# Optimization experiments

Measured on AMD Instinct MI355X. Metric: run time of the kernel, lower is better.

The kernel has to match this reference:

```python
import jax, jax.numpy as jnp
import numpy as np

HEAD_NUM = 8
ATT_DIM = 64
NUM_UNITS = HEAD_NUM * ATT_DIM  # 512
B, T, D = 8, 1024, NUM_UNITS
NEG_BIG = -2.0**32 + 1.0


def _sinusoidal_table(max_len, num_hidden):
    P = np.zeros((1, max_len, num_hidden), dtype=np.float32)
    X = np.arange(max_len, dtype=np.float32).reshape(-1, 1) / np.power(
        10000.0, np.arange(0, num_hidden, 2, dtype=np.float32) / num_hidden)
    P[:, :, 0::2] = np.sin(X)
    P[:, :, 1::2] = np.cos(X)
    return P


def setup_inputs() -> dict:
    key = jax.random.key(0)
    ks = jax.random.split(key, 8)
    w_scale = 0.02
    return {
        "queries": jax.random.normal(ks[0], (B, T, D), dtype=jnp.float32),
        "keys": jax.random.normal(ks[1], (B, T, D), dtype=jnp.float32),
        "query_masks": jnp.ones((B, T), dtype=jnp.float32),
        "key_masks": jnp.ones((B, T), dtype=jnp.float32),
        "pos_table": jnp.asarray(_sinusoidal_table(T, D)),
        "W_Query": jax.random.normal(ks[2], (D, D), dtype=jnp.float32) * w_scale,
        "W_key": jax.random.normal(ks[3], (D, D), dtype=jnp.float32) * w_scale,
        "W_Value": jax.random.normal(ks[4], (D, D), dtype=jnp.float32) * w_scale,
        "fw1": jax.random.normal(ks[5], (D, 4 * D), dtype=jnp.float32) * w_scale,
        "fw2": jax.random.normal(ks[6], (4 * D, D), dtype=jnp.float32) * w_scale,
    }


def reference(queries, keys, query_masks, key_masks, pos_table,
              W_Query, W_key, W_Value, fw1, fw2):
    h, dh = HEAD_NUM, ATT_DIM
    pe_scale = jnp.asarray(NUM_UNITS ** 0.5, dtype=queries.dtype)
    pos = pos_table[:, :queries.shape[1], :] * pe_scale  # scale=True
    q_in = queries + pos
    k_in = keys + pos

    q = jnp.einsum('btd,de->bte', q_in, W_Query)
    k = jnp.einsum('btd,de->bte', k_in, W_key)
    # Faithful to source: values computed from the projected keys.
    v = jnp.einsum('btd,de->bte', k, W_Value)

    # split heads: (B,T,h*dh) -> (h,B,T,dh)
    def heads(x):
        return x.reshape(B, T, h, dh).transpose(2, 0, 1, 3)
    qh, kh, vh = heads(q), heads(k), heads(v)

    scores = jnp.einsum('hbqd,hbkd->hbqk', qh, kh) / (dh ** 0.5)
    # key padding mask
    scores = jnp.where(key_masks[None, :, None, :] == 1.0, scores, NEG_BIG)
    # blinding: mask the diagonal
    eye = jnp.eye(T, dtype=bool)
    scores = jnp.where(eye[None, None, :, :], NEG_BIG, scores)
    attn = jax.nn.softmax(scores, axis=-1)
    attn = attn * query_masks[None, :, :, None]

    out = jnp.einsum('hbqk,hbkd->hbqd', attn, vh)
    result = out.transpose(1, 2, 0, 3).reshape(B, T, D)  # merge heads

    result = result + q_in  # residual (use_res, queries after PE)

    # feed-forward with residual
    hidden = jax.nn.relu(jnp.einsum('btd,df->btf', result, fw1))
    ffn = jnp.einsum('btf,fd->btd', hidden, fw2)
    result = result + ffn

    # output_type == 'mean'
    return jnp.mean(result, axis=1, keepdims=True)  # (B,1,D)
```

## Files before the change

kernel.cpp:

```cpp
#include <hip/hip_runtime.h>


typedef __bf16 bf16x8 __attribute__((ext_vector_type(8)));
typedef __bf16 bf16x4 __attribute__((ext_vector_type(4)));
typedef float f32x4 __attribute__((ext_vector_type(4)));
typedef unsigned short u16x8 __attribute__((ext_vector_type(8)));
typedef unsigned short u16x4 __attribute__((ext_vector_type(4)));

#define MFMA_BF16(a, b, c) __builtin_amdgcn_mfma_f32_16x16x32_bf16((a), (b), (c), 0, 0, 0)
#define NEGBIG (-4294967295.0f)
#define QSCALE 0.18033688011112042f
#define EXP2(x) __builtin_amdgcn_exp2f(x)

#define GLL16(g, l)                                                                 \
    __builtin_amdgcn_global_load_lds((__attribute__((address_space(1))) void*)(g),  \
                                     (__attribute__((address_space(3))) void*)(l),  \
                                     16, 0, 0)

static __device__ __forceinline__ unsigned short f2bf(float f) {
    __bf16 h = (__bf16)f;
    return __builtin_bit_cast(unsigned short, h);
}
static __device__ __forceinline__ float bf2f(unsigned short h) {
    return __builtin_bit_cast(float, ((unsigned int)h) << 16);
}

__global__ __launch_bounds__(256) void prep_wconv_kernel(
    const float* __restrict__ q, const float* __restrict__ k, const float* __restrict__ pos,
    unsigned short* __restrict__ qo, unsigned short* __restrict__ ko,
    const float* __restrict__ w0, const float* __restrict__ w1, const float* __restrict__ w2,
    const float* __restrict__ w3, const float* __restrict__ w4,
    unsigned short* __restrict__ o0, unsigned short* __restrict__ o1, unsigned short* __restrict__ o2,
    unsigned short* __restrict__ o3, unsigned short* __restrict__ o4,
    unsigned short* __restrict__ wkp)
{
    int id = blockIdx.x;
    if (id < 4096) {
        size_t i = ((size_t)id * 256 + threadIdx.x) * 4;
        size_t td = i & (size_t)(1024 * 512 - 1);
        float4 qv = *(const float4*)(q + i);
        float4 kv = *(const float4*)(k + i);
        float4 pv = *(const float4*)(pos + td);
        const float S = 22.627416997969522f;
        u16x4 qr, kr;
        qr[0] = f2bf(qv.x + pv.x * S); qr[1] = f2bf(qv.y + pv.y * S);
        qr[2] = f2bf(qv.z + pv.z * S); qr[3] = f2bf(qv.w + pv.w * S);
        kr[0] = f2bf(kv.x + pv.x * S); kr[1] = f2bf(kv.y + pv.y * S);
        kr[2] = f2bf(kv.z + pv.z * S); kr[3] = f2bf(kv.w + pv.w * S);
        *(u16x4*)(qo + i) = qr;
        *(u16x4*)(ko + i) = kr;
        return;
    }
    id -= 4096;
    const float* in; unsigned short* out; int K, N, kt, nt; bool dup = false;
    if (id < 768) {
        int m = id >> 8; id &= 255;
        in  = (m == 0) ? w0 : ((m == 1) ? w1 : w2);
        out = (m == 0) ? o0 : ((m == 1) ? o1 : o2);
        dup = (m == 1);
        K = 512; N = 512; kt = id >> 4; nt = id & 15;
    } else if (id < 1792) {
        id -= 768; in = w3; out = o3; K = 512; N = 2048; kt = id >> 6; nt = id & 63;
    } else {
        id -= 1792; in = w4; out = o4; K = 2048; N = 512; kt = id >> 4; nt = id & 15;
    }
    int k0 = kt * 32, n0 = nt * 32;
    __shared__ float tile[32][33];
    int tx = threadIdx.x & 31, ty = threadIdx.x >> 5;
#pragma unroll
    for (int i = 0; i < 32; i += 8) {
        float v = in[(size_t)(k0 + ty + i) * N + n0 + tx];
        tile[ty + i][tx] = v;
        if (dup) wkp[(size_t)(k0 + ty + i) * 512 + n0 + tx] = f2bf(v);
    }
    __syncthreads();
#pragma unroll
    for (int i = 0; i < 32; i += 8)
        out[(size_t)(n0 + ty + i) * K + k0 + tx] = f2bf(tile[tx][ty + i]);
}

__global__ __launch_bounds__(256) void gemm64(
    const unsigned short* __restrict__ A, const unsigned short* __restrict__ Bt,
    unsigned short* __restrict__ C, int N, int K)
{
    __shared__ unsigned short As[64 * 32];
    __shared__ unsigned short Bs[64 * 32];
    const int tid = threadIdx.x;
    const int wave = tid >> 6, lane = tid & 63;
    const int g = lane >> 4, lr = lane & 15;
    const int wm = (wave >> 1) * 32, wn = (wave & 1) * 32;
    const size_t bm = (size_t)blockIdx.x * 64, bn = (size_t)blockIdx.y * 64;
    const int row = tid >> 2, kc = (tid & 3) * 8;
    const unsigned short* Ap = A + (bm + row) * (size_t)K + kc;
    const unsigned short* Bp = Bt + (bn + row) * (size_t)K + kc;
    unsigned short* AsW = As + tid * 8;
    unsigned short* BsW = Bs + tid * 8;

    f32x4 acc[2][2] = {};
    for (int k0 = 0; k0 < K; k0 += 32) {
        __syncthreads();
        GLL16(Ap + k0, AsW);
        GLL16(Bp + k0, BsW);
        __syncthreads();
        bf16x8 af[2], bfr[2];
#pragma unroll
        for (int t = 0; t < 2; ++t) {
            af[t]  = *(const bf16x8*)&As[(wm + t * 16 + lr) * 32 + g * 8];
            bfr[t] = *(const bf16x8*)&Bs[(wn + t * 16 + lr) * 32 + g * 8];
        }
#pragma unroll
        for (int i = 0; i < 2; ++i)
#pragma unroll
            for (int j = 0; j < 2; ++j)
                acc[i][j] = MFMA_BF16(af[i], bfr[j], acc[i][j]);
    }
#pragma unroll
    for (int i = 0; i < 2; ++i)
#pragma unroll
        for (int j = 0; j < 2; ++j) {
            size_t rr = bm + wm + i * 16 + g * 4;
            size_t cc = bn + wn + j * 16 + lr;
#pragma unroll
            for (int r = 0; r < 4; ++r)
                C[(rr + r) * (size_t)N + cc] = f2bf(acc[i][j][r]);
        }
}

static __device__ __forceinline__ void gemm_core(
    const unsigned short* __restrict__ A,
    const unsigned short* __restrict__ Bt,
    unsigned short* __restrict__ C,
    int N, int K, int mode,
    unsigned short* As, unsigned short* Bs, int bx, int by)
{
    const int tid = threadIdx.x;
    const int wave = tid >> 6, lane = tid & 63;
    const int g = lane >> 4, lr = lane & 15;
    const int wm = (wave >> 1) * 64, wn = (wave & 1) * 64;
    const size_t bm = (size_t)bx * 128, bn = (size_t)by * 128;

    const int srow = tid >> 2, skc = (tid & 3) * 8;
    const unsigned short* Ap = A + (bm + srow) * (size_t)K + skc;
    const unsigned short* Bp = Bt + (bn + srow) * (size_t)K + skc;
    unsigned short* AsW = As + tid * 8;
    unsigned short* BsW = Bs + tid * 8;

    f32x4 acc[4][4] = {};
    for (int k0 = 0; k0 < K; k0 += 32) {
        __syncthreads();
        GLL16(Ap + k0, AsW);
        GLL16(Ap + (size_t)64 * K + k0, AsW + 2048);
        GLL16(Bp + k0, BsW);
        GLL16(Bp + (size_t)64 * K + k0, BsW + 2048);
        __syncthreads();
        bf16x8 af[4], bfr[4];
#pragma unroll
        for (int t = 0; t < 4; ++t) {
            af[t]  = *(const bf16x8*)&As[(wm + t * 16 + lr) * 32 + g * 8];
            bfr[t] = *(const bf16x8*)&Bs[(wn + t * 16 + lr) * 32 + g * 8];
        }
#pragma unroll
        for (int rt = 0; rt < 4; ++rt)
#pragma unroll
            for (int ct = 0; ct < 4; ++ct)
                acc[rt][ct] = MFMA_BF16(af[rt], bfr[ct], acc[rt][ct]);
    }

#pragma unroll
    for (int rt = 0; rt < 4; ++rt)
#pragma unroll
        for (int ct = 0; ct < 4; ++ct) {
            size_t row = bm + wm + rt * 16 + g * 4;
            size_t col = bn + wn + ct * 16 + lr;
#pragma unroll
            for (int r = 0; r < 4; ++r) {
                float x = acc[rt][ct][r];
                if (mode == 2) x *= QSCALE;
                C[(row + r) * (size_t)N + col] = f2bf(x);
            }
        }
}

__global__ __launch_bounds__(256, 2) void proj3_kernel(
    const unsigned short* __restrict__ q_in, const unsigned short* __restrict__ k_in,
    const unsigned short* __restrict__ wqt, const unsigned short* __restrict__ wkt,
    const unsigned short* __restrict__ wkvt,
    unsigned short* __restrict__ qb, unsigned short* __restrict__ kb,
    unsigned short* __restrict__ vb)
{
    __shared__ unsigned short As[128 * 32];
    __shared__ unsigned short Bs[128 * 32];
    const unsigned short *A, *Bt; unsigned short* C; int mode = 0;
    switch (blockIdx.z) {
        case 0:  A = q_in; Bt = wqt;  C = qb; mode = 2; break;
        case 1:  A = k_in; Bt = wkt;  C = kb; break;
        default: A = k_in; Bt = wkvt; C = vb; break;
    }
    gemm_core(A, Bt, C, 512, 512, mode, As, Bs, blockIdx.x, blockIdx.y);
}

__global__ __launch_bounds__(256, 2) void ffn1_mean(
    const unsigned short* __restrict__ A,
    const unsigned short* __restrict__ Bt,
    float* __restrict__ hmean)
{
    __shared__ unsigned short As[128 * 32];
    __shared__ unsigned short Bs[128 * 32];
    const int tid = threadIdx.x;
    const int wave = tid >> 6, lane = tid & 63;
    const int g = lane >> 4, lr = lane & 15;
    const int wm = (wave >> 1) * 64, wn = (wave & 1) * 64;
    const size_t bm = (size_t)blockIdx.x * 128, bn = (size_t)blockIdx.y * 128;

    const int srow = tid >> 2, skc = (tid & 3) * 8;
    const unsigned short* Ap = A + (bm + srow) * (size_t)512 + skc;
    const unsigned short* Bp = Bt + (bn + srow) * (size_t)512 + skc;
    unsigned short* AsW = As + tid * 8;
    unsigned short* BsW = Bs + tid * 8;

    f32x4 acc[4][4] = {};
    for (int k0 = 0; k0 < 512; k0 += 32) {
        __syncthreads();
        GLL16(Ap + k0, AsW);
        GLL16(Ap + (size_t)64 * 512 + k0, AsW + 2048);
        GLL16(Bp + k0, BsW);
        GLL16(Bp + (size_t)64 * 512 + k0, BsW + 2048);
        __syncthreads();
        bf16x8 af[4], bfr[4];
#pragma unroll
        for (int t = 0; t < 4; ++t) {
            af[t]  = *(const bf16x8*)&As[(wm + t * 16 + lr) * 32 + g * 8];
            bfr[t] = *(const bf16x8*)&Bs[(wn + t * 16 + lr) * 32 + g * 8];
        }
#pragma unroll
        for (int rt = 0; rt < 4; ++rt)
#pragma unroll
            for (int ct = 0; ct < 4; ++ct)
                acc[rt][ct] = MFMA_BF16(af[rt], bfr[ct], acc[rt][ct]);
    }

    const int b = blockIdx.x >> 3;
#pragma unroll
    for (int ct = 0; ct < 4; ++ct) {
        float s = 0.f;
#pragma unroll
        for (int rt = 0; rt < 4; ++rt)
#pragma unroll
            for (int r = 0; r < 4; ++r) s += fmaxf(acc[rt][ct][r], 0.f);
        s += __shfl_xor(s, 16, 64);
        s += __shfl_xor(s, 32, 64);
        if (g == 0)
            atomicAdd(hmean + b * 2048 + bn + wn + ct * 16 + lr, s);
    }
}

__global__ __launch_bounds__(64) void ffn2_small(
    const float* __restrict__ hmean, const unsigned short* __restrict__ fw2t,
    float* __restrict__ out)
{
    const int b = blockIdx.x;
    const int d = blockIdx.y * 64 + threadIdx.x;
    const float* hm = hmean + b * 2048;
    const unsigned short* wr = fw2t + (size_t)d * 2048;
    float acc = 0.f;
    for (int f = 0; f < 2048; f += 8) {
        u16x8 w = *(const u16x8*)(wr + f);
#pragma unroll
        for (int j = 0; j < 8; ++j) acc += hm[f + j] * bf2f(w[j]);
    }
    out[b * 512 + d] += acc * (1.0f / 1024.0f);
}

__global__ __launch_bounds__(512, 4) void attn_kernel(
    const unsigned short* __restrict__ Q,
    const unsigned short* __restrict__ Kp,
    const unsigned short* __restrict__ V,
    const float* __restrict__ queries,
    const float* __restrict__ pos,
    const float* __restrict__ kmask,
    const float* __restrict__ qmask,
    unsigned short* __restrict__ Res,
    float* __restrict__ out)
{
    __shared__ unsigned short Ks[64 * 72];
    __shared__ unsigned short Vts[64 * 72];
    __shared__ unsigned short Ps[8][16 * 72];
    __shared__ float kbias[1024];
    const int tid = threadIdx.x, wave = tid >> 6, lane = tid & 63;
    const int g = lane >> 4, lr = lane & 15;
    const int b = blockIdx.y >> 3, h = blockIdx.y & 7;
    const int qg = blockIdx.x * 128 + wave * 16 + lr;

    for (int i = tid; i < 1024; i += 512)
        kbias[i] = (kmask[b * 1024 + i] == 1.0f) ? 0.f : NEGBIG;

    bf16x8 aq0, aq1;
    {
        const unsigned short* qp = Q + ((size_t)(b * 1024 + qg)) * 512 + h * 64 + g * 8;
        aq0 = *(const bf16x8*)qp;
        aq1 = *(const bf16x8*)(qp + 32);
    }
    const float qm = qmask[b * 1024 + qg];

    float m_run = -3.0e38f, l_run = 0.f;
    f32x4 o[4] = {};

    const unsigned short* kbase = Kp + ((size_t)(b * 1024)) * 512 + h * 64;
    const unsigned short* vbase = V + ((size_t)(b * 1024)) * 512 + h * 64;

    const int half = tid >> 8;
    const int skey = (tid & 255) >> 2, sd = (tid & 3) * 16;
    const int vk0 = (tid & 15) * 4, vd0 = ((tid >> 4) & 15) * 4;

    u16x8 kr0, kr1; u16x4 vr[4];
    if (half) {
        const unsigned short* kp = kbase + (size_t)skey * 512 + sd;
        kr0 = *(const u16x8*)kp; kr1 = *(const u16x8*)(kp + 8);
    } else {
        const unsigned short* vp = vbase + (size_t)vk0 * 512 + vd0;
#pragma unroll
        for (int j = 0; j < 4; ++j) vr[j] = *(const u16x4*)(vp + (size_t)j * 512);
    }

    for (int j0 = 0; j0 < 1024; j0 += 64) {
        __syncthreads();
        if (half) {
            *(u16x8*)&Ks[skey * 72 + sd] = kr0;
            *(u16x8*)&Ks[skey * 72 + sd + 8] = kr1;
        } else {
#pragma unroll
            for (int i = 0; i < 4; ++i) {
                u16x4 w = { vr[0][i], vr[1][i], vr[2][i], vr[3][i] };
                *(u16x4*)&Vts[(vd0 + i) * 72 + vk0] = w;
            }
        }
        __syncthreads();
        if (j0 + 64 < 1024) {
            if (half) {
                const unsigned short* kp = kbase + (size_t)(j0 + 64 + skey) * 512 + sd;
                kr0 = *(const u16x8*)kp; kr1 = *(const u16x8*)(kp + 8);
            } else {
                const unsigned short* vp = vbase + (size_t)(j0 + 64 + vk0) * 512 + vd0;
#pragma unroll
                for (int j = 0; j < 4; ++j) vr[j] = *(const u16x4*)(vp + (size_t)j * 512);
            }
        }

        f32x4 s[4];
#pragma unroll
        for (int ct = 0; ct < 4; ++ct) {
            bf16x8 ka = *(const bf16x8*)&Ks[(ct * 16 + lr) * 72 + g * 8];
            bf16x8 kc = *(const bf16x8*)&Ks[(ct * 16 + lr) * 72 + 32 + g * 8];
            f32x4 z = {};
            z = MFMA_BF16(ka, aq0, z);
            s[ct] = MFMA_BF16(kc, aq1, z);
        }

#pragma unroll
        for (int ct = 0; ct < 4; ++ct)
            s[ct] += *(const f32x4*)&kbias[j0 + ct * 16 + g * 4];
        if (((qg ^ j0) & ~63) == 0) {
#pragma unroll
            for (int ct = 0; ct < 4; ++ct) {
                unsigned diff = (unsigned)(qg - (j0 + ct * 16 + g * 4));
                if (diff < 4u) s[ct][diff] = NEGBIG;
            }
        }
        float rmax = -3.0e38f;
#pragma unroll
        for (int ct = 0; ct < 4; ++ct)
#pragma unroll
            for (int r = 0; r < 4; ++r) rmax = fmaxf(rmax, s[ct][r]);
        rmax = fmaxf(rmax, __shfl_xor(rmax, 16, 64));
        rmax = fmaxf(rmax, __shfl_xor(rmax, 32, 64));

        float mn = fmaxf(m_run, rmax);
        float alpha = EXP2(m_run - mn);
        m_run = mn;
        float psum = 0.f;
#pragma unroll
        for (int ct = 0; ct < 4; ++ct) {
            f32x4 p;
#pragma unroll
            for (int r = 0; r < 4; ++r) { p[r] = EXP2(s[ct][r] - mn); psum += p[r]; }
            bf16x4 pk = { (__bf16)p[0], (__bf16)p[1], (__bf16)p[2], (__bf16)p[3] };
            *(bf16x4*)&Ps[wave][lr * 72 + ct * 16 + g * 4] = pk;
        }
        psum += __shfl_xor(psum, 16, 64);
        psum += __shfl_xor(psum, 32, 64);
        l_run = l_run * alpha + psum;
#pragma unroll
        for (int dt = 0; dt < 4; ++dt) o[dt] *= alpha;

        bf16x8 p0 = *(const bf16x8*)&Ps[wave][lr * 72 + g * 8];
        bf16x8 p1 = *(const bf16x8*)&Ps[wave][lr * 72 + 32 + g * 8];
#pragma unroll
        for (int dt = 0; dt < 4; ++dt) {
            bf16x8 va = *(const bf16x8*)&Vts[(dt * 16 + lr) * 72 + g * 8];
            bf16x8 vc = *(const bf16x8*)&Vts[(dt * 16 + lr) * 72 + 32 + g * 8];
            o[dt] = MFMA_BF16(va, p0, o[dt]);
            o[dt] = MFMA_BF16(vc, p1, o[dt]);
        }
    }

    const float inv_l = 1.0f / l_run;
    const float S = 22.627416997969522f;
    float vals[4][4];
#pragma unroll
    for (int dt = 0; dt < 4; ++dt) {
        size_t col = (size_t)h * 64 + dt * 16 + g * 4;
        size_t idx = ((size_t)(b * 1024 + qg)) * 512 + col;
        f32x4 qv = *(const f32x4*)&queries[idx];
        f32x4 pv = *(const f32x4*)&pos[(size_t)qg * 512 + col];
        u16x4 wr;
#pragma unroll
        for (int r = 0; r < 4; ++r) {
            float v = o[dt][r] * inv_l * qm + qv[r] + pv[r] * S;
            vals[dt][r] = v;
            wr[r] = f2bf(v);
        }
        *(u16x4*)&Res[idx] = wr;
    }

    __syncthreads();
    float* red = kbias;
#pragma unroll
    for (int dt = 0; dt < 4; ++dt)
#pragma unroll
        for (int r = 0; r < 4; ++r) {
            float x = vals[dt][r];
            x += __shfl_xor(x, 1, 64);
            x += __shfl_xor(x, 2, 64);
            x += __shfl_xor(x, 4, 64);
            x += __shfl_xor(x, 8, 64);
            if (lr == 0) red[wave * 64 + dt * 16 + g * 4 + r] = x;
        }
    __syncthreads();
    if (tid < 64) {
        float s = 0.f;
#pragma unroll
        for (int w = 0; w < 8; ++w) s += red[w * 64 + tid];
        atomicAdd(out + b * 512 + h * 64 + tid, s * (1.0f / 1024.0f));
    }
}

extern "C" void kernel_launch(void* const* d_in, const int* in_sizes, int n_in,
                              void* d_out, int out_size, void* d_ws, size_t ws_size,
                              hipStream_t stream)
{
    (void)in_sizes; (void)n_in; (void)out_size; (void)ws_size;
    const float* queries     = (const float*)d_in[0];
    const float* keys        = (const float*)d_in[1];
    const float* query_masks = (const float*)d_in[2];
    const float* key_masks   = (const float*)d_in[3];
    const float* pos_table   = (const float*)d_in[4];
    const float* W_Query     = (const float*)d_in[5];
    const float* W_key       = (const float*)d_in[6];
    const float* W_Value     = (const float*)d_in[7];
    const float* fw1         = (const float*)d_in[8];
    const float* fw2         = (const float*)d_in[9];
    float* out = (float*)d_out;

    unsigned short* ws = (unsigned short*)d_ws;
    const size_t NE = (size_t)8 * 1024 * 512;
    unsigned short* q_in   = ws;
    unsigned short* k_in   = ws + NE;
    unsigned short* qb     = ws + 2 * NE;
    unsigned short* kb     = ws + 3 * NE;
    unsigned short* vb     = ws + 4 * NE;
    unsigned short* result = q_in;
    unsigned short* wqt    = ws + 6 * NE;
    unsigned short* wkt    = wqt + 512 * 512;
    unsigned short* wvt    = wkt + 512 * 512;
    unsigned short* fw1t   = wvt + 512 * 512;
    unsigned short* fw2t   = fw1t + 2048 * 512;
    unsigned short* wkp    = fw2t + 2048 * 512;
    unsigned short* wkvt   = wkp + 512 * 512;
    float*          hmean  = (float*)(wkvt + 512 * 512);

    hipMemsetAsync(d_out, 0, 8 * 512 * sizeof(float), stream);
    hipMemsetAsync(hmean, 0, 8 * 2048 * sizeof(float), stream);
    prep_wconv_kernel<<<6912, 256, 0, stream>>>(queries, keys, pos_table, q_in, k_in,
                                                W_Query, W_key, W_Value, fw1, fw2,
                                                wqt, wkt, wvt, fw1t, fw2t, wkp);
    gemm64<<<dim3(8, 8), 256, 0, stream>>>(wvt, wkp, wkvt, 512, 512);
    proj3_kernel<<<dim3(64, 4, 3), 256, 0, stream>>>(q_in, k_in, wqt, wkt, wkvt, qb, kb, vb);
    attn_kernel<<<dim3(8, 64), 512, 0, stream>>>(qb, kb, vb, queries, pos_table,
                                                 key_masks, query_masks, result, out);
    ffn1_mean<<<dim3(64, 16), 256, 0, stream>>>(result, fw1t, hmean);
    ffn2_small<<<dim3(8, 8), 64, 0, stream>>>(hmean, fw2t, out);
}
```

Measured before the change: 252.1 us.

## Double-buffer K/V tiles in attention, split prep kernel, parallelize ffn2 reduction

The attention loop now double-buffers K and V in shared memory. This needs only one barrier per iteration instead of two, and the next tile's register-to-LDS store overlaps the current compute. Launch bounds drop from 4 to 2 blocks per SM because LDS use grows. The fused prep/weight-conversion kernel is split into two separate launches. ffn2_small now splits the 2048-long reduction across four waves with vector loads and a shared-memory sum, to raise parallelism in that tiny kernel.

```diff
diff --git a/kernel.cpp b/kernel.cpp
--- a/kernel.cpp
+++ b/kernel.cpp
@@ -25,9 +25,27 @@
     return __builtin_bit_cast(float, ((unsigned int)h) << 16);
 }
 
-__global__ __launch_bounds__(256) void prep_wconv_kernel(
-    const float* __restrict__ q, const float* __restrict__ k, const float* __restrict__ pos,
-    unsigned short* __restrict__ qo, unsigned short* __restrict__ ko,
+__global__ __launch_bounds__(256) void prep_kernel(
+    const float* __restrict__ q, const float* __restrict__ k,
+    const float* __restrict__ pos,
+    unsigned short* __restrict__ qo, unsigned short* __restrict__ ko)
+{
+    size_t i = ((size_t)blockIdx.x * 256 + threadIdx.x) * 4;
+    size_t td = i & (size_t)(1024 * 512 - 1);
+    float4 qv = *(const float4*)(q + i);
+    float4 kv = *(const float4*)(k + i);
+    float4 pv = *(const float4*)(pos + td);
+    const float S = 22.627416997969522f;
+    u16x4 qr, kr;
+    qr[0] = f2bf(qv.x + pv.x * S); qr[1] = f2bf(qv.y + pv.y * S);
+    qr[2] = f2bf(qv.z + pv.z * S); qr[3] = f2bf(qv.w + pv.w * S);
+    kr[0] = f2bf(kv.x + pv.x * S); kr[1] = f2bf(kv.y + pv.y * S);
+    kr[2] = f2bf(kv.z + pv.z * S); kr[3] = f2bf(kv.w + pv.w * S);
+    *(u16x4*)(qo + i) = qr;
+    *(u16x4*)(ko + i) = kr;
+}
+
+__global__ __launch_bounds__(256) void wconv_kernel(
     const float* __restrict__ w0, const float* __restrict__ w1, const float* __restrict__ w2,
     const float* __restrict__ w3, const float* __restrict__ w4,
     unsigned short* __restrict__ o0, unsigned short* __restrict__ o1, unsigned short* __restrict__ o2,
@@ -35,23 +53,6 @@
     unsigned short* __restrict__ wkp)
 {
     int id = blockIdx.x;
-    if (id < 4096) {
-        size_t i = ((size_t)id * 256 + threadIdx.x) * 4;
-        size_t td = i & (size_t)(1024 * 512 - 1);
-        float4 qv = *(const float4*)(q + i);
-        float4 kv = *(const float4*)(k + i);
-        float4 pv = *(const float4*)(pos + td);
-        const float S = 22.627416997969522f;
-        u16x4 qr, kr;
-        qr[0] = f2bf(qv.x + pv.x * S); qr[1] = f2bf(qv.y + pv.y * S);
-        qr[2] = f2bf(qv.z + pv.z * S); qr[3] = f2bf(qv.w + pv.w * S);
-        kr[0] = f2bf(kv.x + pv.x * S); kr[1] = f2bf(kv.y + pv.y * S);
-        kr[2] = f2bf(kv.z + pv.z * S); kr[3] = f2bf(kv.w + pv.w * S);
-        *(u16x4*)(qo + i) = qr;
-        *(u16x4*)(ko + i) = kr;
-        return;
-    }
-    id -= 4096;
     const float* in; unsigned short* out; int K, N, kt, nt; bool dup = false;
     if (id < 768) {
         int m = id >> 8; id &= 255;
@@ -254,24 +255,34 @@
     }
 }
 
-__global__ __launch_bounds__(64) void ffn2_small(
+__global__ __launch_bounds__(256) void ffn2_small(
     const float* __restrict__ hmean, const unsigned short* __restrict__ fw2t,
     float* __restrict__ out)
 {
+    __shared__ float red[256];
     const int b = blockIdx.x;
-    const int d = blockIdx.y * 64 + threadIdx.x;
-    const float* hm = hmean + b * 2048;
-    const unsigned short* wr = fw2t + (size_t)d * 2048;
+    const int d = blockIdx.y * 64 + (threadIdx.x & 63);
+    const int fs = (threadIdx.x >> 6) * 512;
+    const float* hm = hmean + b * 2048 + fs;
+    const unsigned short* wr = fw2t + (size_t)d * 2048 + fs;
     float acc = 0.f;
-    for (int f = 0; f < 2048; f += 8) {
+    for (int f = 0; f < 512; f += 8) {
         u16x8 w = *(const u16x8*)(wr + f);
-#pragma unroll
-        for (int j = 0; j < 8; ++j) acc += hm[f + j] * bf2f(w[j]);
-    }
-    out[b * 512 + d] += acc * (1.0f / 1024.0f);
-}
-
-__global__ __launch_bounds__(512, 4) void attn_kernel(
+        f32x4 h0 = *(const f32x4*)(hm + f);
+        f32x4 h1 = *(const f32x4*)(hm + f + 4);
+        acc += h0[0] * bf2f(w[0]) + h0[1] * bf2f(w[1]) + h0[2] * bf2f(w[2]) + h0[3] * bf2f(w[3])
+             + h1[0] * bf2f(w[4]) + h1[1] * bf2f(w[5]) + h1[2] * bf2f(w[6]) + h1[3] * bf2f(w[7]);
+    }
+    red[threadIdx.x] = acc;
+    __syncthreads();
+    if (threadIdx.x < 64) {
+        float s = red[threadIdx.x] + red[threadIdx.x + 64] +
+                  red[threadIdx.x + 128] + red[threadIdx.x + 192];
+        out[b * 512 + d] += s * (1.0f / 1024.0f);
+    }
+}
+
+__global__ __launch_bounds__(512, 2) void attn_kernel(
     const unsigned short* __restrict__ Q,
     const unsigned short* __restrict__ Kp,
     const unsigned short* __restrict__ V,
@@ -282,8 +293,8 @@
     unsigned short* __restrict__ Res,
     float* __restrict__ out)
 {
-    __shared__ unsigned short Ks[64 * 72];
-    __shared__ unsigned short Vts[64 * 72];
+    __shared__ unsigned short Ks[2][64 * 72];
+    __shared__ unsigned short Vts[2][64 * 72];
     __shared__ unsigned short Ps[8][16 * 72];
     __shared__ float kbias[1024];
     const int tid = threadIdx.x, wave = tid >> 6, lane = tid & 63;
@@ -321,36 +332,36 @@
 #pragma unroll
         for (int j = 0; j < 4; ++j) vr[j] = *(const u16x4*)(vp + (size_t)j * 512);
     }
-
-    for (int j0 = 0; j0 < 1024; j0 += 64) {
-        __syncthreads();
-        if (half) {
-            *(u16x8*)&Ks[skey * 72 + sd] = kr0;
-            *(u16x8*)&Ks[skey * 72 + sd + 8] = kr1;
-        } else {
-#pragma unroll
-            for (int i = 0; i < 4; ++i) {
-                u16x4 w = { vr[0][i], vr[1][i], vr[2][i], vr[3][i] };
-                *(u16x4*)&Vts[(vd0 + i) * 72 + vk0] = w;
-            }
-        }
-        __syncthreads();
-        if (j0 + 64 < 1024) {
-            if (half) {
-                const unsigned short* kp = kbase + (size_t)(j0 + 64 + skey) * 512 + sd;
-                kr0 = *(const u16x8*)kp; kr1 = *(const u16x8*)(kp + 8);
-            } else {
-                const unsigned short* vp = vbase + (size_t)(j0 + 64 + vk0) * 512 + vd0;
-#pragma unroll
-                for (int j = 0; j < 4; ++j) vr[j] = *(const u16x4*)(vp + (size_t)j * 512);
-            }
-        }
+    if (half) {
+        *(u16x8*)&Ks[0][skey * 72 + sd] = kr0;
+        *(u16x8*)&Ks[0][skey * 72 + sd + 8] = kr1;
+    } else {
+#pragma unroll
+        for (int i = 0; i < 4; ++i) {
+            u16x4 w = { vr[0][i], vr[1][i], vr[2][i], vr[3][i] };
+            *(u16x4*)&Vts[0][(vd0 + i) * 72 + vk0] = w;
+        }
+    }
+    if (half) {
+        const unsigned short* kp = kbase + (size_t)(64 + skey) * 512 + sd;
+        kr0 = *(const u16x8*)kp; kr1 = *(const u16x8*)(kp + 8);
+    } else {
+        const unsigned short* vp = vbase + (size_t)(64 + vk0) * 512 + vd0;
+#pragma unroll
+        for (int j = 0; j < 4; ++j) vr[j] = *(const u16x4*)(vp + (size_t)j * 512);
+    }
+    __syncthreads();
+
+    for (int it = 0; it < 16; ++it) {
+        const int j0 = it * 64;
+        const unsigned short* Kc = Ks[it & 1];
+        const unsigned short* Vc = Vts[it & 1];
 
         f32x4 s[4];
 #pragma unroll
         for (int ct = 0; ct < 4; ++ct) {
-            bf16x8 ka = *(const bf16x8*)&Ks[(ct * 16 + lr) * 72 + g * 8];
-            bf16x8 kc = *(const bf16x8*)&Ks[(ct * 16 + lr) * 72 + 32 + g * 8];
+            bf16x8 ka = *(const bf16x8*)&Kc[(ct * 16 + lr) * 72 + g * 8];
+            bf16x8 kc = *(const bf16x8*)&Kc[(ct * 16 + lr) * 72 + 32 + g * 8];
             f32x4 z = {};
             z = MFMA_BF16(ka, aq0, z);
             s[ct] = MFMA_BF16(kc, aq1, z);
@@ -396,11 +407,38 @@
         bf16x8 p1 = *(const bf16x8*)&Ps[wave][lr * 72 + 32 + g * 8];
 #pragma unroll
         for (int dt = 0; dt < 4; ++dt) {
-            bf16x8 va = *(const bf16x8*)&Vts[(dt * 16 + lr) * 72 + g * 8];
-            bf16x8 vc = *(const bf16x8*)&Vts[(dt * 16 + lr) * 72 + 32 + g * 8];
+            bf16x8 va = *(const bf16x8*)&Vc[(dt * 16 + lr) * 72 + g * 8];
+            bf16x8 vc = *(const bf16x8*)&Vc[(dt * 16 + lr) * 72 + 32 + g * 8];
             o[dt] = MFMA_BF16(va, p0, o[dt]);
             o[dt] = MFMA_BF16(vc, p1, o[dt]);
         }
+
+        if (it + 1 < 16) {
+            unsigned short* Kn = Ks[(it + 1) & 1];
+            unsigned short* Vn = Vts[(it + 1) & 1];
+            if (half) {
+                *(u16x8*)&Kn[skey * 72 + sd] = kr0;
+                *(u16x8*)&Kn[skey * 72 + sd + 8] = kr1;
+            } else {
+#pragma unroll
+                for (int i = 0; i < 4; ++i) {
+                    u16x4 w = { vr[0][i], vr[1][i], vr[2][i], vr[3][i] };
+                    *(u16x4*)&Vn[(vd0 + i) * 72 + vk0] = w;
+                }
+            }
+        }
+        if (it + 2 < 16) {
+            const int jn = (it + 2) * 64;
+            if (half) {
+                const unsigned short* kp = kbase + (size_t)(jn + skey) * 512 + sd;
+                kr0 = *(const u16x8*)kp; kr1 = *(const u16x8*)(kp + 8);
+            } else {
+                const unsigned short* vp = vbase + (size_t)(jn + vk0) * 512 + vd0;
+#pragma unroll
+                for (int j = 0; j < 4; ++j) vr[j] = *(const u16x4*)(vp + (size_t)j * 512);
+            }
+        }
+        __syncthreads();
     }
 
     const float inv_l = 1.0f / l_run;
@@ -422,7 +460,6 @@
         *(u16x4*)&Res[idx] = wr;
     }
 
-    __syncthreads();
     float* red = kbias;
 #pragma unroll
     for (int dt = 0; dt < 4; ++dt)
@@ -480,13 +517,13 @@
 
     hipMemsetAsync(d_out, 0, 8 * 512 * sizeof(float), stream);
     hipMemsetAsync(hmean, 0, 8 * 2048 * sizeof(float), stream);
-    prep_wconv_kernel<<<6912, 256, 0, stream>>>(queries, keys, pos_table, q_in, k_in,
-                                                W_Query, W_key, W_Value, fw1, fw2,
-                                                wqt, wkt, wvt, fw1t, fw2t, wkp);
+    prep_kernel<<<4096, 256, 0, stream>>>(queries, keys, pos_table, q_in, k_in);
+    wconv_kernel<<<2816, 256, 0, stream>>>(W_Query, W_key, W_Value, fw1, fw2,
+                                           wqt, wkt, wvt, fw1t, fw2t, wkp);
     gemm64<<<dim3(8, 8), 256, 0, stream>>>(wvt, wkp, wkvt, 512, 512);
     proj3_kernel<<<dim3(64, 4, 3), 256, 0, stream>>>(q_in, k_in, wqt, wkt, wkvt, qb, kb, vb);
     attn_kernel<<<dim3(8, 64), 512, 0, stream>>>(qb, kb, vb, queries, pos_table,
                                                  key_masks, query_masks, result, out);
     ffn1_mean<<<dim3(64, 16), 256, 0, stream>>>(result, fw1t, hmean);
-    ffn2_small<<<dim3(8, 8), 64, 0, stream>>>(hmean, fw2t, out);
-}
+    ffn2_small<<<dim3(8, 8), 256, 0, stream>>>(hmean, fw2t, out);
+}
```

Result: faster. 212.4 us (-15.8%).
